# Kernel tuning notes

Hardware: AMD Instinct MI355X
Metric: run time of the kernel (lower is better)

The kernel has to match this reference:

```python
import jax, jax.numpy as jnp
import numpy as np

N_VOX = 150000
GRID = 256
C_IN = 32
C_OUT = 64
EPS = 1e-5


def _build_neighbor_idx(n=N_VOX, g=GRID, seed=0):
    # Build a submanifold-conv rulebook: for each of 27 kernel offsets and each
    # output voxel, the index of the input voxel at that offset, or -1 if absent.
    rng = np.random.default_rng(seed)
    lin = rng.choice(g ** 3, size=n, replace=False).astype(np.int64)
    coords = np.stack(np.unravel_index(lin, (g, g, g)), axis=1)  # [N,3]
    order = np.argsort(lin)
    sorted_keys = lin[order]
    offs = np.array([[dx, dy, dz] for dx in (-1, 0, 1) for dy in (-1, 0, 1) for dz in (-1, 0, 1)], dtype=np.int64)  # [27,3]
    nbr = np.full((27, n), -1, dtype=np.int32)
    for k in range(27):
        nc = coords + offs[k]  # neighbor coords [N,3]
        valid = np.all((nc >= 0) & (nc < g), axis=1)
        nkey = (nc[:, 0] * g + nc[:, 1]) * g + nc[:, 2]
        pos = np.searchsorted(sorted_keys, nkey)
        pos_c = np.clip(pos, 0, n - 1)
        found = valid & (sorted_keys[pos_c] == nkey)
        nbr[k] = np.where(found, order[pos_c].astype(np.int32), -1)
    return jnp.asarray(nbr)


def setup_inputs() -> dict:
    key = jax.random.key(0)
    k1, k2, k3, k4 = jax.random.split(key, 4)
    features = jax.random.normal(k1, (N_VOX, C_IN), dtype=jnp.float32)
    weight = jax.random.normal(k2, (27, C_IN, C_OUT), dtype=jnp.float32) * 0.05
    gamma = jax.random.uniform(k3, (C_OUT,), dtype=jnp.float32, minval=0.5, maxval=1.5)
    beta = jax.random.normal(k4, (C_OUT,), dtype=jnp.float32) * 0.1
    neighbor_idx = _build_neighbor_idx()
    return {"features": features, "weight": weight, "gamma": gamma, "beta": beta, "neighbor_idx": neighbor_idx}


def reference(features, weight, gamma, beta, neighbor_idx):
    # --- SubMConv3d via rulebook gather -> GEMM -> (implicit) scatter ---
    safe_idx = jnp.maximum(neighbor_idx, 0)            # [K,N]
    gathered = features[safe_idx]                      # [K,N,Cin]
    mask = (neighbor_idx >= 0)[..., None]              # [K,N,1]
    gathered = jnp.where(mask, gathered, jnp.zeros((), features.dtype))
    out = jnp.einsum('knc,kcd->nd', gathered, weight)  # [N,Cout]
    # --- BatchNorm1d (training-mode batch stats, biased var) + ReLU ---
    mean = jnp.mean(out, axis=0)
    var = jnp.mean(jnp.square(out - mean), axis=0)
    normed = (out - mean) * jax.lax.rsqrt(var + EPS)
    return jax.nn.relu(normed * gamma + beta)
```

## Files before the change

### kernel.cpp

```cpp
#include <hip/hip_runtime.h>

#define NV    150000
#define CIN   32
#define COUT  64
#define EPSF  1e-5f
#define NCOPY 16

#define NTHR   256
#define NTILES (NV / 16)
#define NBLK1  ((NTILES + 3) / 4)

#define NBLK2  2344
#define TOTAL4 ((long)NV * COUT / 4)
#define STRIDE2 ((long)NBLK2 * NTHR)

typedef short  bf16x8 __attribute__((ext_vector_type(8)));
typedef float  f32x4  __attribute__((ext_vector_type(4)));

__device__ __forceinline__ short f2bf(float x) {
    union { float f; unsigned u; } c; c.f = x;
    return (short)((c.u + 0x7FFFu + ((c.u >> 16) & 1u)) >> 16);
}

__global__ __launch_bounds__(NTHR) void k_conv(
    const float* __restrict__ feat,
    const float* __restrict__ weight,
    const int*   __restrict__ nbr,
    float*       __restrict__ out,
    float*       __restrict__ gstats)
{
    const int tid  = threadIdx.x;
    const int lane = tid & 63;
    const int quad = lane >> 4;
    const int lm   = lane & 15;
    const int wid  = blockIdx.x * 4 + (tid >> 6);

    f32x4 ssum = {0.f, 0.f, 0.f, 0.f};
    f32x4 qsum = {0.f, 0.f, 0.f, 0.f};
    f32x4 acc[4] = {{0.f,0.f,0.f,0.f},{0.f,0.f,0.f,0.f},{0.f,0.f,0.f,0.f},{0.f,0.f,0.f,0.f}};

    const bool have_tile = (wid < NTILES);
    const int v0 = have_tile ? wid * 16 : 0;

    if (have_tile) {
        int sidx[7];
#pragma unroll
        for (int it = 0; it < 7; ++it) {
            const int item = lane + it * 64;
            int idx = -1;
            if (item < 416) {
                const int kp = item >> 4;
                const int k  = kp + (kp >= 13);
                idx = nbr[(long)k * NV + v0 + (item & 15)];
            }
            sidx[it] = idx;
        }

        {
            const float4* fp = (const float4*)(feat + (long)(v0 + lm) * CIN + quad * 8);
            const float4 fa = fp[0];
            const float4 fb = fp[1];
            bf16x8 afr;
            afr[0] = f2bf(fa.x); afr[1] = f2bf(fa.y); afr[2] = f2bf(fa.z); afr[3] = f2bf(fa.w);
            afr[4] = f2bf(fb.x); afr[5] = f2bf(fb.y); afr[6] = f2bf(fb.z); afr[7] = f2bf(fb.w);
#pragma unroll
            for (int b = 0; b < 4; ++b) {
                const float* wsrc = weight + 13 * CIN * COUT + (quad * 8) * COUT + b * 16 + lm;
                bf16x8 bfr;
#pragma unroll
                for (int j = 0; j < 8; ++j) bfr[j] = f2bf(wsrc[j * COUT]);
                acc[b] = __builtin_amdgcn_mfma_f32_16x16x32_bf16(afr, bfr, acc[b], 0, 0, 0);
            }
        }

        unsigned int kmask = 0u;
#pragma unroll
        for (int it = 0; it < 7; ++it) {
            const unsigned long long m = __ballot(sidx[it] >= 0);
            kmask |= ((m & 0xFFFFull)         ? 1u : 0u) << (it * 4 + 0);
            kmask |= (((m >> 16) & 0xFFFFull) ? 1u : 0u) << (it * 4 + 1);
            kmask |= (((m >> 32) & 0xFFFFull) ? 1u : 0u) << (it * 4 + 2);
            kmask |= ((m >> 48)               ? 1u : 0u) << (it * 4 + 3);
        }

        while (kmask) {
            const int kpA = __ffs(kmask) - 1;
            kmask &= kmask - 1u;
            int kpB = -1;
            if (kmask) { kpB = __ffs(kmask) - 1; kmask &= kmask - 1u; }
            const int kA = kpA + (kpA >= 13);
            const int kB = (kpB >= 0) ? (kpB + (kpB >= 13)) : kA;

            const int idxA = nbr[(long)kA * NV + v0 + lm];
            const int idxB = (kpB >= 0) ? nbr[(long)kB * NV + v0 + lm] : -1;

            const float4* fpA = (const float4*)(feat + (long)(idxA < 0 ? 0 : idxA) * CIN + quad * 8);
            const float4* fpB = (const float4*)(feat + (long)(idxB < 0 ? 0 : idxB) * CIN + quad * 8);
            float4 gaA = fpA[0], gbA = fpA[1];
            float4 gaB = fpB[0], gbB = fpB[1];
            if (idxA < 0) { gaA = make_float4(0.f,0.f,0.f,0.f); gbA = make_float4(0.f,0.f,0.f,0.f); }
            if (idxB < 0) { gaB = make_float4(0.f,0.f,0.f,0.f); gbB = make_float4(0.f,0.f,0.f,0.f); }

            bf16x8 naA, naB;
            naA[0] = f2bf(gaA.x); naA[1] = f2bf(gaA.y); naA[2] = f2bf(gaA.z); naA[3] = f2bf(gaA.w);
            naA[4] = f2bf(gbA.x); naA[5] = f2bf(gbA.y); naA[6] = f2bf(gbA.z); naA[7] = f2bf(gbA.w);
            naB[0] = f2bf(gaB.x); naB[1] = f2bf(gaB.y); naB[2] = f2bf(gaB.z); naB[3] = f2bf(gaB.w);
            naB[4] = f2bf(gbB.x); naB[5] = f2bf(gbB.y); naB[6] = f2bf(gbB.z); naB[7] = f2bf(gbB.w);

            const float* wkA = weight + (long)kA * CIN * COUT + (quad * 8) * COUT + lm;
            const float* wkB = weight + (long)kB * CIN * COUT + (quad * 8) * COUT + lm;
#pragma unroll
            for (int b = 0; b < 4; ++b) {
                bf16x8 wbA, wbB;
#pragma unroll
                for (int j = 0; j < 8; ++j) {
                    wbA[j] = f2bf(wkA[j * COUT + b * 16]);
                    wbB[j] = f2bf(wkB[j * COUT + b * 16]);
                }
                acc[b] = __builtin_amdgcn_mfma_f32_16x16x32_bf16(naA, wbA, acc[b], 0, 0, 0);
                acc[b] = __builtin_amdgcn_mfma_f32_16x16x32_bf16(naB, wbB, acc[b], 0, 0, 0);
            }
        }

#pragma unroll
        for (int b = 0; b < 4; ++b) {
            const float r0 = acc[b][0], r1 = acc[b][1], r2 = acc[b][2], r3 = acc[b][3];
            out[(long)(v0 + quad * 4 + 0) * COUT + b * 16 + lm] = r0;
            out[(long)(v0 + quad * 4 + 1) * COUT + b * 16 + lm] = r1;
            out[(long)(v0 + quad * 4 + 2) * COUT + b * 16 + lm] = r2;
            out[(long)(v0 + quad * 4 + 3) * COUT + b * 16 + lm] = r3;
            ssum[b] += r0 + r1 + r2 + r3;
            qsum[b] += r0 * r0 + r1 * r1 + r2 * r2 + r3 * r3;
        }
    }

#pragma unroll
    for (int off = 16; off < 64; off <<= 1) {
#pragma unroll
        for (int b = 0; b < 4; ++b) {
            ssum[b] += __shfl_xor(ssum[b], off);
            qsum[b] += __shfl_xor(qsum[b], off);
        }
    }

    __shared__ float ls[4][128];
    const int wv = tid >> 6;
    if (quad == 0) {
#pragma unroll
        for (int b = 0; b < 4; ++b) {
            ls[wv][b * 16 + lm]      = ssum[b];
            ls[wv][64 + b * 16 + lm] = qsum[b];
        }
    }
    __syncthreads();
    if (tid < 128) {
        const float v = ls[0][tid] + ls[1][tid] + ls[2][tid] + ls[3][tid];
        atomicAdd(gstats + (blockIdx.x & (NCOPY - 1)) * 128 + tid, v);
    }
}

__global__ __launch_bounds__(NTHR) void k_norm(
    float*       __restrict__ out,
    const float* __restrict__ gstats,
    const float* __restrict__ gamma,
    const float* __restrict__ beta)
{
    __shared__ float sscale[COUT];
    __shared__ float sshift[COUT];
    const int tid = threadIdx.x;
    if (tid < COUT) {
        float s = 0.f, q = 0.f;
#pragma unroll
        for (int cp = 0; cp < NCOPY; ++cp) {
            s += gstats[cp * 128 + tid];
            q += gstats[cp * 128 + 64 + tid];
        }
        const float inv_n = 1.f / (float)NV;
        const float mean = s * inv_n;
        float var = q * inv_n - mean * mean;
        var = fmaxf(var, 0.f);
        const float rstd = rsqrtf(var + EPSF);
        const float sc = gamma[tid] * rstd;
        sscale[tid] = sc;
        sshift[tid] = beta[tid] - mean * sc;
    }
    __syncthreads();

    const int g4 = (tid & 15) * 4;
    const float4 SC = make_float4(sscale[g4], sscale[g4 + 1], sscale[g4 + 2], sscale[g4 + 3]);
    const float4 SH = make_float4(sshift[g4], sshift[g4 + 1], sshift[g4 + 2], sshift[g4 + 3]);

    float4* o4 = (float4*)out;
    const long base = (long)blockIdx.x * NTHR + tid;

    float4 v0 = o4[base];
    float4 v1 = o4[base + STRIDE2];
    float4 v2 = o4[base + 2 * STRIDE2];
    const long i3 = base + 3 * STRIDE2;
    const bool has3 = (i3 < TOTAL4);
    float4 v3 = has3 ? o4[i3] : make_float4(0.f, 0.f, 0.f, 0.f);

    v0.x = fmaxf(v0.x * SC.x + SH.x, 0.f); v0.y = fmaxf(v0.y * SC.y + SH.y, 0.f);
    v0.z = fmaxf(v0.z * SC.z + SH.z, 0.f); v0.w = fmaxf(v0.w * SC.w + SH.w, 0.f);
    v1.x = fmaxf(v1.x * SC.x + SH.x, 0.f); v1.y = fmaxf(v1.y * SC.y + SH.y, 0.f);
    v1.z = fmaxf(v1.z * SC.z + SH.z, 0.f); v1.w = fmaxf(v1.w * SC.w + SH.w, 0.f);
    v2.x = fmaxf(v2.x * SC.x + SH.x, 0.f); v2.y = fmaxf(v2.y * SC.y + SH.y, 0.f);
    v2.z = fmaxf(v2.z * SC.z + SH.z, 0.f); v2.w = fmaxf(v2.w * SC.w + SH.w, 0.f);
    v3.x = fmaxf(v3.x * SC.x + SH.x, 0.f); v3.y = fmaxf(v3.y * SC.y + SH.y, 0.f);
    v3.z = fmaxf(v3.z * SC.z + SH.z, 0.f); v3.w = fmaxf(v3.w * SC.w + SH.w, 0.f);

    o4[base] = v0;
    o4[base + STRIDE2] = v1;
    o4[base + 2 * STRIDE2] = v2;
    if (has3) o4[i3] = v3;
}

extern "C" void kernel_launch(void* const* d_in, const int* in_sizes, int n_in,
                              void* d_out, int out_size, void* d_ws, size_t ws_size,
                              hipStream_t stream) {
    const float* feat   = (const float*)d_in[0];
    const float* weight = (const float*)d_in[1];
    const float* gamma  = (const float*)d_in[2];
    const float* beta   = (const float*)d_in[3];
    const int*   nbr    = (const int*)d_in[4];
    float* out = (float*)d_out;

    float* gstats = (float*)d_ws;

    hipMemsetAsync(d_ws, 0, NCOPY * 128 * sizeof(float), stream);

    k_conv<<<NBLK1, NTHR, 0, stream>>>(feat, weight, nbr, out, gstats);
    k_norm<<<NBLK2, NTHR, 0, stream>>>(out, gstats, gamma, beta);
}
```

Measured before the change: 127.9 us.

## Pre-convert features and weights to bf16 fragments in a prep kernel

Adds a prep kernel that converts the feature matrix to packed bf16 and lays the weights out as per-lane MFMA B fragments in workspace, and zeroes the stats there instead of using a memset. The conv kernel then gathers 16-byte bf16 rows and loads weight fragments with single uint4 reads, with no per-element conversion. Neighbor indices are taken from the already-loaded sidx registers via shuffles instead of being reloaded from global memory. This halves gather bytes and removes conversion ALU work, at the cost of an extra kernel pass over the features.

New measurement: 120.6 us. -5.7%, faster.

```diff
diff --git a/kernel.cpp b/kernel.cpp
--- a/kernel.cpp
+++ b/kernel.cpp
@@ -14,21 +14,77 @@
 #define TOTAL4 ((long)NV * COUT / 4)
 #define STRIDE2 ((long)NBLK2 * NTHR)
 
+#define FEAT_T   (NV * CIN / 8)
+#define FEATBLK  ((FEAT_T + NTHR - 1) / NTHR)
+#define PREPBLK  (FEATBLK + 27 + 1)
+
+#define WS_WFRAG  9600000
+#define WS_GSTATS 9710592
+
 typedef short  bf16x8 __attribute__((ext_vector_type(8)));
 typedef float  f32x4  __attribute__((ext_vector_type(4)));
 
-__device__ __forceinline__ short f2bf(float x) {
-    union { float f; unsigned u; } c; c.f = x;
-    return (short)((c.u + 0x7FFFu + ((c.u >> 16) & 1u)) >> 16);
-}
-
-__global__ __launch_bounds__(NTHR) void k_conv(
+union u4bf { uint4 u; bf16x8 h; };
+
+__device__ __forceinline__ unsigned pack_bf2(float a, float b) {
+    union { float f; unsigned u; } ca, cb;
+    ca.f = a; cb.f = b;
+    const unsigned lo = (ca.u + 0x7FFFu + ((ca.u >> 16) & 1u)) >> 16;
+    const unsigned hi = (cb.u + 0x7FFFu + ((cb.u >> 16) & 1u)) & 0xFFFF0000u;
+    return lo | hi;
+}
+
+__global__ __launch_bounds__(NTHR) void k_prep(
     const float* __restrict__ feat,
     const float* __restrict__ weight,
+    char*        __restrict__ ws)
+{
+    const int b = blockIdx.x;
+    if (b < FEATBLK) {
+        const int t = b * NTHR + threadIdx.x;
+        if (t < FEAT_T) {
+            const float4* src = (const float4*)(feat) + t * 2;
+            const float4 f0 = src[0];
+            const float4 f1 = src[1];
+            uint4 o;
+            o.x = pack_bf2(f0.x, f0.y);
+            o.y = pack_bf2(f0.z, f0.w);
+            o.z = pack_bf2(f1.x, f1.y);
+            o.w = pack_bf2(f1.z, f1.w);
+            ((uint4*)ws)[t] = o;
+        }
+    } else if (b < FEATBLK + 27) {
+        const int k    = b - FEATBLK;
+        const int bb   = threadIdx.x >> 6;
+        const int lane = threadIdx.x & 63;
+        const int quad = lane >> 4;
+        const int lm   = lane & 15;
+        const float* wsrc = weight + (long)k * CIN * COUT + (quad * 8) * COUT + bb * 16 + lm;
+        float f[8];
+#pragma unroll
+        for (int j = 0; j < 8; ++j) f[j] = wsrc[j * COUT];
+        uint4 o;
+        o.x = pack_bf2(f[0], f[1]);
+        o.y = pack_bf2(f[2], f[3]);
+        o.z = pack_bf2(f[4], f[5]);
+        o.w = pack_bf2(f[6], f[7]);
+        ((uint4*)(ws + WS_WFRAG))[(k * 4 + bb) * 64 + lane] = o;
+    } else {
+        float* gs = (float*)(ws + WS_GSTATS);
+#pragma unroll
+        for (int i = 0; i < 8; ++i) gs[threadIdx.x + i * NTHR] = 0.f;
+    }
+}
+
+__global__ __launch_bounds__(NTHR) void k_conv(
+    const char*  __restrict__ ws_ro,
     const int*   __restrict__ nbr,
     float*       __restrict__ out,
     float*       __restrict__ gstats)
 {
+    const uint4* fb = (const uint4*)ws_ro;
+    const uint4* wf = (const uint4*)(ws_ro + WS_WFRAG);
+
     const int tid  = threadIdx.x;
     const int lane = tid & 63;
     const int quad = lane >> 4;
@@ -57,19 +113,11 @@
         }
 
         {
-            const float4* fp = (const float4*)(feat + (long)(v0 + lm) * CIN + quad * 8);
-            const float4 fa = fp[0];
-            const float4 fb = fp[1];
-            bf16x8 afr;
-            afr[0] = f2bf(fa.x); afr[1] = f2bf(fa.y); afr[2] = f2bf(fa.z); afr[3] = f2bf(fa.w);
-            afr[4] = f2bf(fb.x); afr[5] = f2bf(fb.y); afr[6] = f2bf(fb.z); afr[7] = f2bf(fb.w);
+            u4bf a; a.u = fb[(v0 + lm) * 4 + quad];
 #pragma unroll
             for (int b = 0; b < 4; ++b) {
-                const float* wsrc = weight + 13 * CIN * COUT + (quad * 8) * COUT + b * 16 + lm;
-                bf16x8 bfr;
-#pragma unroll
-                for (int j = 0; j < 8; ++j) bfr[j] = f2bf(wsrc[j * COUT]);
-                acc[b] = __builtin_amdgcn_mfma_f32_16x16x32_bf16(afr, bfr, acc[b], 0, 0, 0);
+                u4bf w; w.u = wf[(13 * 4 + b) * 64 + lane];
+                acc[b] = __builtin_amdgcn_mfma_f32_16x16x32_bf16(a.h, w.h, acc[b], 0, 0, 0);
             }
         }
 
@@ -91,34 +139,37 @@
             const int kA = kpA + (kpA >= 13);
             const int kB = (kpB >= 0) ? (kpB + (kpB >= 13)) : kA;
 
-            const int idxA = nbr[(long)kA * NV + v0 + lm];
-            const int idxB = (kpB >= 0) ? nbr[(long)kB * NV + v0 + lm] : -1;
-
-            const float4* fpA = (const float4*)(feat + (long)(idxA < 0 ? 0 : idxA) * CIN + quad * 8);
-            const float4* fpB = (const float4*)(feat + (long)(idxB < 0 ? 0 : idxB) * CIN + quad * 8);
-            float4 gaA = fpA[0], gbA = fpA[1];
-            float4 gaB = fpB[0], gbB = fpB[1];
-            if (idxA < 0) { gaA = make_float4(0.f,0.f,0.f,0.f); gbA = make_float4(0.f,0.f,0.f,0.f); }
-            if (idxB < 0) { gaB = make_float4(0.f,0.f,0.f,0.f); gbB = make_float4(0.f,0.f,0.f,0.f); }
-
-            bf16x8 naA, naB;
-            naA[0] = f2bf(gaA.x); naA[1] = f2bf(gaA.y); naA[2] = f2bf(gaA.z); naA[3] = f2bf(gaA.w);
-            naA[4] = f2bf(gbA.x); naA[5] = f2bf(gbA.y); naA[6] = f2bf(gbA.z); naA[7] = f2bf(gbA.w);
-            naB[0] = f2bf(gaB.x); naB[1] = f2bf(gaB.y); naB[2] = f2bf(gaB.z); naB[3] = f2bf(gaB.w);
-            naB[4] = f2bf(gbB.x); naB[5] = f2bf(gbB.y); naB[6] = f2bf(gbB.z); naB[7] = f2bf(gbB.w);
-
-            const float* wkA = weight + (long)kA * CIN * COUT + (quad * 8) * COUT + lm;
-            const float* wkB = weight + (long)kB * CIN * COUT + (quad * 8) * COUT + lm;
+            int rawA, rawB;
+            switch (kpA >> 2) {
+                case 0: rawA = sidx[0]; break; case 1: rawA = sidx[1]; break;
+                case 2: rawA = sidx[2]; break; case 3: rawA = sidx[3]; break;
+                case 4: rawA = sidx[4]; break; case 5: rawA = sidx[5]; break;
+                default: rawA = sidx[6]; break;
+            }
+            const int kpB2 = (kpB >= 0) ? kpB : kpA;
+            switch (kpB2 >> 2) {
+                case 0: rawB = sidx[0]; break; case 1: rawB = sidx[1]; break;
+                case 2: rawB = sidx[2]; break; case 3: rawB = sidx[3]; break;
+                case 4: rawB = sidx[4]; break; case 5: rawB = sidx[5]; break;
+                default: rawB = sidx[6]; break;
+            }
+            const int idxA = __shfl(rawA, ((kpA & 3) << 4) | lm);
+            int idxB = __shfl(rawB, ((kpB2 & 3) << 4) | lm);
+            if (kpB < 0) idxB = -1;
+
+            u4bf aA, aB;
+            aA.u = fb[(long)(idxA < 0 ? 0 : idxA) * 4 + quad];
+            aB.u = fb[(long)(idxB < 0 ? 0 : idxB) * 4 + quad];
+            if (idxA < 0) aA.u = make_uint4(0u, 0u, 0u, 0u);
+            if (idxB < 0) aB.u = make_uint4(0u, 0u, 0u, 0u);
+
 #pragma unroll
             for (int b = 0; b < 4; ++b) {
-                bf16x8 wbA, wbB;
-#pragma unroll
-                for (int j = 0; j < 8; ++j) {
-                    wbA[j] = f2bf(wkA[j * COUT + b * 16]);
-                    wbB[j] = f2bf(wkB[j * COUT + b * 16]);
-                }
-                acc[b] = __builtin_amdgcn_mfma_f32_16x16x32_bf16(naA, wbA, acc[b], 0, 0, 0);
-                acc[b] = __builtin_amdgcn_mfma_f32_16x16x32_bf16(naB, wbB, acc[b], 0, 0, 0);
+                u4bf wA, wB;
+                wA.u = wf[(kA * 4 + b) * 64 + lane];
+                wB.u = wf[(kB * 4 + b) * 64 + lane];
+                acc[b] = __builtin_amdgcn_mfma_f32_16x16x32_bf16(aA.h, wA.h, acc[b], 0, 0, 0);
+                acc[b] = __builtin_amdgcn_mfma_f32_16x16x32_bf16(aB.h, wB.h, acc[b], 0, 0, 0);
             }
         }
 
@@ -225,10 +276,10 @@
     const int*   nbr    = (const int*)d_in[4];
     float* out = (float*)d_out;
 
-    float* gstats = (float*)d_ws;
-
-    hipMemsetAsync(d_ws, 0, NCOPY * 128 * sizeof(float), stream);
-
-    k_conv<<<NBLK1, NTHR, 0, stream>>>(feat, weight, nbr, out, gstats);
+    char*  ws     = (char*)d_ws;
+    float* gstats = (float*)(ws + WS_GSTATS);
+
+    k_prep<<<PREPBLK, NTHR, 0, stream>>>(feat, weight, ws);
+    k_conv<<<NBLK1, NTHR, 0, stream>>>(ws, nbr, out, gstats);
     k_norm<<<NBLK2, NTHR, 0, stream>>>(out, gstats, gamma, beta);
 }
```
